# Kernel tuning notes

Hardware: AMD Instinct MI355X
Metric: run time of the kernel (lower is better)

Reference implementation:

```python
import jax, jax.numpy as jnp
import numpy as np

N_NODES = 100000
N_EDGES = 1600000
D_IN, D_HID, D_OUT = 256, 256, 128


def setup_inputs() -> dict:
    key = jax.random.key(0)
    k1, k2, k3, k4, k5, k6 = jax.random.split(key, 6)
    x = jax.random.normal(k1, (N_NODES, D_IN), dtype=jnp.float32)
    edge_index = jax.random.randint(k2, (2, N_EDGES), 0, N_NODES, dtype=jnp.int64)
    W1 = jax.random.normal(k3, (D_IN, D_HID), dtype=jnp.float32) / np.sqrt(D_IN)
    b1 = jax.random.normal(k4, (D_HID,), dtype=jnp.float32) * 0.01
    W2 = jax.random.normal(k5, (D_HID, D_OUT), dtype=jnp.float32) / np.sqrt(D_HID)
    b2 = jax.random.normal(k6, (D_OUT,), dtype=jnp.float32) * 0.01
    return {"x": x, "edge_index": edge_index, "W1": W1, "b1": b1, "W2": W2, "b2": b2}


def _gcn_conv(x, src, dst, W, b, n_nodes):
    # PyG GCNConv: linear transform, add self-loops, symmetric normalization,
    # scatter-add aggregation, bias.
    h = x @ W                                         # [N, D_out]
    # degree including self-loop (edge weight 1)
    deg = jax.ops.segment_sum(jnp.ones((src.shape[0],), h.dtype), dst,
                              num_segments=n_nodes) + 1.0
    dinv = jax.lax.rsqrt(deg)                         # [N]
    norm = dinv[src] * dinv[dst]                      # [E]
    msg = h[src] * norm[:, None]                      # [E, D_out] gather + scale
    agg = jax.ops.segment_sum(msg, dst, num_segments=n_nodes)
    # self-loop contribution: norm_ii = dinv_i^2
    agg = agg + h * (dinv * dinv)[:, None]
    return agg + b


def reference(x, edge_index, W1, b1, W2, b2):
    src, dst = edge_index[0], edge_index[1]
    n = x.shape[0]
    h = _gcn_conv(x, src, dst, W1, b1, n)
    h = jax.nn.relu(h)
    out = _gcn_conv(h, src, dst, W2, b2, n)
    return out
```

## Files before the change

kernel.cpp:

```cpp
#include <hip/hip_runtime.h>

#define N_NODES 100000
#define N_EDGES 1600000
#define D_IN 256
#define D_HID 256
#define D_OUT 128
#define SLOTS 96

typedef unsigned int u32;
typedef unsigned short u16;
typedef __attribute__((ext_vector_type(8))) short bf16x8;
typedef __attribute__((ext_vector_type(8))) unsigned short u16x8;
typedef __attribute__((ext_vector_type(4))) float f32x4;

__device__ __forceinline__ u16 f2bf(float v) {
    u32 u = __float_as_uint(v);
    u32 r = (u + 0x7fffu + ((u >> 16) & 1u)) >> 16;
    return (u16)r;
}
__device__ __forceinline__ float bf2f(u16 b) {
    return __uint_as_float(((u32)b) << 16);
}

__global__ __launch_bounds__(256) void prep_kernel(
    const float* __restrict__ x, u16* __restrict__ xhi,
    const float* __restrict__ W1, u16* __restrict__ w1hi, u16* __restrict__ w1lo,
    const float* __restrict__ W2, u16* __restrict__ w2hi, u16* __restrict__ w2lo,
    const int* __restrict__ src, const int* __restrict__ dst,
    int* __restrict__ deg, int* __restrict__ slot) {
    const int tid = blockIdx.x * 256 + threadIdx.x;
    const int stride = gridDim.x * 256;

    const int n4 = N_NODES * D_IN / 4;
    for (int i = tid; i < n4; i += stride) {
        const float4 v = ((const float4*)x)[i];
        ushort4 h;
        h.x = f2bf(v.x);
        h.y = f2bf(v.y);
        h.z = f2bf(v.z);
        h.w = f2bf(v.w);
        ((ushort4*)xhi)[i] = h;
    }
    for (int i = tid; i < D_IN * D_HID; i += stride) {
        const int k = i / D_HID, n = i - k * D_HID;
        const float v = W1[i];
        const u16 h = f2bf(v);
        w1hi[(size_t)n * D_IN + k] = h;
        w1lo[(size_t)n * D_IN + k] = f2bf(v - bf2f(h));
    }
    for (int i = tid; i < D_HID * D_OUT; i += stride) {
        const int k = i / D_OUT, n = i - k * D_OUT;
        const float v = W2[i];
        const u16 h = f2bf(v);
        w2hi[(size_t)n * D_HID + k] = h;
        w2lo[(size_t)n * D_HID + k] = f2bf(v - bf2f(h));
    }
    for (int e = tid; e < N_EDGES; e += stride) {
        const int s = src[e];
        const int d = dst[e];
        const int pos = atomicAdd(&deg[d], 1);
        if (pos < SLOTS) slot[(size_t)d * SLOTS + pos] = s;
    }
}

__global__ void dinv_kernel(const int* __restrict__ deg, float* __restrict__ dinv, int n) {
    int i = blockIdx.x * blockDim.x + threadIdx.x;
    if (i < n) dinv[i] = rsqrtf((float)deg[i] + 1.0f);
}

template <bool ASPLIT>
__global__ __launch_bounds__(256) void gemm_split(
    const u16* __restrict__ Ahi, const u16* __restrict__ Alo,
    const u16* __restrict__ Bhi, const u16* __restrict__ Blo,
    u16* __restrict__ Cb, int M, int N, int K) {
    constexpr int ABYTES = ASPLIT ? 16384 : 8192;
    __shared__ char lds[2][ABYTES + 16384];
    const int t = threadIdx.x;
    const int wave = t >> 6;
    const int lane = t & 63;
    const int wm = wave >> 1, wn = wave & 1;
    const int mBase = blockIdx.x * 128;
    const int nBase = blockIdx.y * 128;

    f32x4 acc[4][4];
#pragma unroll
    for (int i = 0; i < 4; ++i)
#pragma unroll
        for (int j = 0; j < 4; ++j) acc[i][j] = (f32x4){0.f, 0.f, 0.f, 0.f};

    const int lr = lane >> 3;
    const int lp = lane & 7;
    const int lc = lp ^ lr;
    const int lr4 = lane >> 2;
    const int lc4 = (lane & 3) ^ (lr4 & 3);

    auto STAGE = [&](int buf, int kt) {
        const int k0 = kt * 32;
        if (ASPLIT) {
            const int coff = k0 + (lc & 3) * 8;
            const u16* aSrc = (lc < 4) ? Ahi : Alo;
#pragma unroll
            for (int q = 0; q < 4; ++q) {
                const int row = wave * 32 + q * 8 + lr;
                int mg = mBase + row;
                if (mg > M - 1) mg = M - 1;
                const u16* s = aSrc + (size_t)mg * K + coff;
                char* d = &lds[buf][(wave * 32 + q * 8) * 128];
                __builtin_amdgcn_global_load_lds(
                    (const __attribute__((address_space(1))) u32*)s,
                    (__attribute__((address_space(3))) u32*)d, 16, 0, 0);
            }
        } else {
            const int coff = k0 + lc4 * 8;
#pragma unroll
            for (int q = 0; q < 2; ++q) {
                const int row = wave * 32 + q * 16 + lr4;
                int mg = mBase + row;
                if (mg > M - 1) mg = M - 1;
                const u16* s = Ahi + (size_t)mg * K + coff;
                char* d = &lds[buf][(wave * 32 + q * 16) * 64];
                __builtin_amdgcn_global_load_lds(
                    (const __attribute__((address_space(1))) u32*)s,
                    (__attribute__((address_space(3))) u32*)d, 16, 0, 0);
            }
        }
        {
            const int coff = k0 + (lc & 3) * 8;
            const u16* bSrc = (lc < 4) ? Bhi : Blo;
#pragma unroll
            for (int q = 0; q < 4; ++q) {
                const int row = wave * 32 + q * 8 + lr;
                const int ng = nBase + row;
                const u16* s = bSrc + (size_t)ng * K + coff;
                char* d = &lds[buf][ABYTES + (wave * 32 + q * 8) * 128];
                __builtin_amdgcn_global_load_lds(
                    (const __attribute__((address_space(1))) u32*)s,
                    (__attribute__((address_space(3))) u32*)d, 16, 0, 0);
            }
        }
    };

    auto COMPUTE = [&](int buf) {
        const char* pa = &lds[buf][0];
        const char* pb = &lds[buf][ABYTES];
        const int lm = lane & 15;
        const int c4 = lane >> 4;
        bf16x8 ah[4], al[4], bh[4], bl[4];
#pragma unroll
        for (int i = 0; i < 4; ++i) {
            const int r = wm * 64 + i * 16 + lm;
            if (ASPLIT) {
                const int s = r & 7;
                ah[i] = *(const bf16x8*)(pa + r * 128 + ((c4) ^ s) * 16);
                al[i] = *(const bf16x8*)(pa + r * 128 + ((c4 + 4) ^ s) * 16);
            } else {
                ah[i] = *(const bf16x8*)(pa + r * 64 + (c4 ^ (r & 3)) * 16);
            }
        }
#pragma unroll
        for (int j = 0; j < 4; ++j) {
            const int r = wn * 64 + j * 16 + lm;
            const int s = r & 7;
            bh[j] = *(const bf16x8*)(pb + r * 128 + ((c4) ^ s) * 16);
            bl[j] = *(const bf16x8*)(pb + r * 128 + ((c4 + 4) ^ s) * 16);
        }
#pragma unroll
        for (int i = 0; i < 4; ++i)
#pragma unroll
            for (int j = 0; j < 4; ++j)
                acc[i][j] = __builtin_amdgcn_mfma_f32_16x16x32_bf16(ah[i], bh[j], acc[i][j], 0, 0, 0);
#pragma unroll
        for (int i = 0; i < 4; ++i)
#pragma unroll
            for (int j = 0; j < 4; ++j)
                acc[i][j] = __builtin_amdgcn_mfma_f32_16x16x32_bf16(ah[i], bl[j], acc[i][j], 0, 0, 0);
        if (ASPLIT) {
#pragma unroll
            for (int i = 0; i < 4; ++i)
#pragma unroll
                for (int j = 0; j < 4; ++j)
                    acc[i][j] = __builtin_amdgcn_mfma_f32_16x16x32_bf16(al[i], bh[j], acc[i][j], 0, 0, 0);
        }
    };

    const int NT = K / 32;
    STAGE(0, 0);
#pragma unroll 1
    for (int kt = 0; kt < NT; ++kt) {
        __syncthreads();
        if (kt + 1 < NT) STAGE((kt + 1) & 1, kt + 1);
        COMPUTE(kt & 1);
        __syncthreads();
    }

    const int lm = lane & 15;
    const int c4 = lane >> 4;
#pragma unroll
    for (int i = 0; i < 4; ++i) {
#pragma unroll
        for (int r = 0; r < 4; ++r) {
            const int row = mBase + wm * 64 + i * 16 + c4 * 4 + r;
            if (row < M) {
#pragma unroll
                for (int j = 0; j < 4; ++j) {
                    const int col = nBase + wn * 64 + j * 16 + lm;
                    Cb[(size_t)row * N + col] = f2bf(acc[i][j][r]);
                }
            }
        }
    }
}

__global__ __launch_bounds__(256) void gather_agg_bf16(const u16* __restrict__ h,
                                                       const int* __restrict__ deg,
                                                       const int* __restrict__ slot,
                                                       const float* __restrict__ dinv,
                                                       const float* __restrict__ bias,
                                                       u16* __restrict__ ob, int n) {
    const int node = blockIdx.x * 8 + (threadIdx.x >> 5);
    const int lane = threadIdx.x & 31;
    if (node >= n) return;
    const float di = dinv[node];
    int dg = deg[node];
    if (dg > SLOTS) dg = SLOTS;
    const int* sp = &slot[(size_t)node * SLOTS];
    const int off = lane * 8;

    float acc[8];
#pragma unroll
    for (int j = 0; j < 8; ++j) acc[j] = 0.f;

    int k = 0;
    for (; k + 1 < dg; k += 2) {
        const int s0 = sp[k];
        const int s1 = sp[k + 1];
        const float n0 = dinv[s0] * di;
        const float n1 = dinv[s1] * di;
        const u16x8 va = *(const u16x8*)&h[(size_t)s0 * 256 + off];
        const u16x8 vb = *(const u16x8*)&h[(size_t)s1 * 256 + off];
#pragma unroll
        for (int j = 0; j < 8; ++j)
            acc[j] += bf2f(va[j]) * n0 + bf2f(vb[j]) * n1;
    }
    if (k < dg) {
        const int s0 = sp[k];
        const float n0 = dinv[s0] * di;
        const u16x8 va = *(const u16x8*)&h[(size_t)s0 * 256 + off];
#pragma unroll
        for (int j = 0; j < 8; ++j) acc[j] += bf2f(va[j]) * n0;
    }

    const float sl = di * di;
    const u16x8 hv = *(const u16x8*)&h[(size_t)node * 256 + off];
    const float4 bv0 = *(const float4*)&bias[off];
    const float4 bv1 = *(const float4*)&bias[off + 4];
    const float bb[8] = {bv0.x, bv0.y, bv0.z, bv0.w, bv1.x, bv1.y, bv1.z, bv1.w};
    u16x8 H;
#pragma unroll
    for (int j = 0; j < 8; ++j)
        H[j] = f2bf(fmaxf(acc[j] + bf2f(hv[j]) * sl + bb[j], 0.f));
    *(u16x8*)&ob[(size_t)node * 256 + off] = H;
}

__global__ __launch_bounds__(256) void gather_agg_out(const u16* __restrict__ h,
                                                      const int* __restrict__ deg,
                                                      const int* __restrict__ slot,
                                                      const float* __restrict__ dinv,
                                                      const float* __restrict__ bias,
                                                      float* __restrict__ outp, int n) {
    const int node = blockIdx.x * 16 + (threadIdx.x >> 4);
    const int lane = threadIdx.x & 15;
    if (node >= n) return;
    const float di = dinv[node];
    int dg = deg[node];
    if (dg > SLOTS) dg = SLOTS;
    const int* sp = &slot[(size_t)node * SLOTS];
    const int off = lane * 8;

    float acc[8];
#pragma unroll
    for (int j = 0; j < 8; ++j) acc[j] = 0.f;

    int k = 0;
    for (; k + 1 < dg; k += 2) {
        const int s0 = sp[k];
        const int s1 = sp[k + 1];
        const float n0 = dinv[s0] * di;
        const float n1 = dinv[s1] * di;
        const u16x8 va = *(const u16x8*)&h[(size_t)s0 * 128 + off];
        const u16x8 vb = *(const u16x8*)&h[(size_t)s1 * 128 + off];
#pragma unroll
        for (int j = 0; j < 8; ++j)
            acc[j] += bf2f(va[j]) * n0 + bf2f(vb[j]) * n1;
    }
    if (k < dg) {
        const int s0 = sp[k];
        const float n0 = dinv[s0] * di;
        const u16x8 va = *(const u16x8*)&h[(size_t)s0 * 128 + off];
#pragma unroll
        for (int j = 0; j < 8; ++j) acc[j] += bf2f(va[j]) * n0;
    }

    const float sl = di * di;
    const u16x8 hv = *(const u16x8*)&h[(size_t)node * 128 + off];
    const float4 bv0 = *(const float4*)&bias[off];
    const float4 bv1 = *(const float4*)&bias[off + 4];
    const float bb[8] = {bv0.x, bv0.y, bv0.z, bv0.w, bv1.x, bv1.y, bv1.z, bv1.w};
    float o[8];
#pragma unroll
    for (int j = 0; j < 8; ++j) o[j] = acc[j] + bf2f(hv[j]) * sl + bb[j];
    float4 o0 = make_float4(o[0], o[1], o[2], o[3]);
    float4 o1 = make_float4(o[4], o[5], o[6], o[7]);
    *(float4*)&outp[(size_t)node * 128 + off] = o0;
    *(float4*)&outp[(size_t)node * 128 + off + 4] = o1;
}

extern "C" void kernel_launch(void* const* d_in, const int* in_sizes, int n_in,
                              void* d_out, int out_size, void* d_ws, size_t ws_size,
                              hipStream_t stream) {
    const float* x  = (const float*)d_in[0];
    const int*   ei = (const int*)d_in[1];
    const float* W1 = (const float*)d_in[2];
    const float* b1 = (const float*)d_in[3];
    const float* W2 = (const float*)d_in[4];
    const float* b2 = (const float*)d_in[5];
    float* out = (float*)d_out;

    const int* src = ei;
    const int* dst = ei + N_EDGES;

    char* ws = (char*)d_ws;
    float* dinv = (float*)(ws + 0x000000);
    int*   deg  = (int*)  (ws + 0x080000);
    u16* wt1hi = (u16*)(ws + 0x200000);
    u16* wt1lo = (u16*)(ws + 0x220000);
    u16* wt2hi = (u16*)(ws + 0x240000);
    u16* wt2lo = (u16*)(ws + 0x250000);
    int* slot  = (int*)(ws + 0x280000);
    const size_t big = 0x2800000;
    u16*   Phi = (u16*)(ws + big);
    u16*   Hb  = (u16*)(ws + big + 51200000);

    hipMemsetAsync(deg, 0, N_NODES * sizeof(int), stream);

    prep_kernel<<<2048, 256, 0, stream>>>(x, Phi, W1, wt1hi, wt1lo,
                                          W2, wt2hi, wt2lo, src, dst, deg, slot);
    dinv_kernel<<<(N_NODES + 255) / 256, 256, 0, stream>>>(deg, dinv, N_NODES);

    {
        dim3 g((N_NODES + 127) / 128, D_HID / 128);
        gemm_split<false><<<g, 256, 0, stream>>>(Phi, (const u16*)nullptr, wt1hi, wt1lo,
                                                 Hb, N_NODES, D_HID, D_IN);
    }
    gather_agg_bf16<<<(N_NODES + 7) / 8, 256, 0, stream>>>(
        Hb, deg, slot, dinv, b1, Phi, N_NODES);

    {
        dim3 g((N_NODES + 127) / 128, D_OUT / 128);
        gemm_split<false><<<g, 256, 0, stream>>>(Phi, (const u16*)nullptr, wt2hi, wt2lo,
                                                 Hb, N_NODES, D_OUT, D_HID);
    }
    gather_agg_out<<<(N_NODES + 15) / 16, 256, 0, stream>>>(
        Hb, deg, slot, dinv, b2, out, N_NODES);
}
```

Measured before the change: 375.4 us.

## Bin edges by destination bucket before slot scatter to localize atomics

Edge-to-slot construction moves out of the prep kernel into a two-pass scheme. Edges are first binned into 1024 destination buckets using shared-memory histograms and one global offset per bucket. A per-bucket kernel then does the degree atomics and slot writes, so they hit a compact node range instead of random addresses across all nodes. It adds two launches, an extra pass over the edges through a binned buffer, and a per-bucket cap of 2048 that could drop edges if a bucket overflows. The unused ASPLIT template path is removed from the GEMM.

```diff
diff --git a/kernel.cpp b/kernel.cpp
--- a/kernel.cpp
+++ b/kernel.cpp
@@ -7,6 +7,11 @@
 #define D_OUT 128
 #define SLOTS 96
 
+#define NB 1024
+#define NPB 98
+#define CAP 2048
+#define BIN_T 8192
+
 typedef unsigned int u32;
 typedef unsigned short u16;
 typedef __attribute__((ext_vector_type(8))) short bf16x8;
@@ -25,9 +30,7 @@
 __global__ __launch_bounds__(256) void prep_kernel(
     const float* __restrict__ x, u16* __restrict__ xhi,
     const float* __restrict__ W1, u16* __restrict__ w1hi, u16* __restrict__ w1lo,
-    const float* __restrict__ W2, u16* __restrict__ w2hi, u16* __restrict__ w2lo,
-    const int* __restrict__ src, const int* __restrict__ dst,
-    int* __restrict__ deg, int* __restrict__ slot) {
+    const float* __restrict__ W2, u16* __restrict__ w2hi, u16* __restrict__ w2lo) {
     const int tid = blockIdx.x * 256 + threadIdx.x;
     const int stride = gridDim.x * 256;
 
@@ -55,11 +58,56 @@
         w2hi[(size_t)n * D_HID + k] = h;
         w2lo[(size_t)n * D_HID + k] = f2bf(v - bf2f(h));
     }
-    for (int e = tid; e < N_EDGES; e += stride) {
-        const int s = src[e];
-        const int d = dst[e];
-        const int pos = atomicAdd(&deg[d], 1);
-        if (pos < SLOTS) slot[(size_t)d * SLOTS + pos] = s;
+}
+
+__global__ __launch_bounds__(256) void bin_kernel(const int* __restrict__ src,
+                                                  const int* __restrict__ dst,
+                                                  int* __restrict__ gcnt,
+                                                  int2* __restrict__ binned, int E) {
+    __shared__ int hist[NB];
+    __shared__ int cur[NB];
+    const int t = threadIdx.x;
+    const int base = blockIdx.x * BIN_T;
+#pragma unroll
+    for (int q = 0; q < NB / 256; ++q) hist[q * 256 + t] = 0;
+    __syncthreads();
+#pragma unroll 4
+    for (int j = 0; j < BIN_T / 256; ++j) {
+        const int e = base + j * 256 + t;
+        if (e < E) atomicAdd(&hist[dst[e] / NPB], 1);
+    }
+    __syncthreads();
+#pragma unroll
+    for (int q = 0; q < NB / 256; ++q) {
+        const int b = q * 256 + t;
+        const int c = hist[b];
+        cur[b] = c ? atomicAdd(&gcnt[b], c) : 0;
+    }
+    __syncthreads();
+#pragma unroll 4
+    for (int j = 0; j < BIN_T / 256; ++j) {
+        const int e = base + j * 256 + t;
+        if (e < E) {
+            const int d = dst[e];
+            const int b = d / NPB;
+            const int r = atomicAdd(&cur[b], 1);
+            if (r < CAP) binned[(size_t)b * CAP + r] = make_int2(src[e], d);
+        }
+    }
+}
+
+__global__ __launch_bounds__(256) void bucket_scatter(const int* __restrict__ gcnt,
+                                                      const int2* __restrict__ binned,
+                                                      int* __restrict__ deg,
+                                                      int* __restrict__ slot) {
+    const int b = blockIdx.x;
+    int cnt = gcnt[b];
+    if (cnt > CAP) cnt = CAP;
+    const int2* ep = &binned[(size_t)b * CAP];
+    for (int i = threadIdx.x; i < cnt; i += 256) {
+        const int2 e = ep[i];
+        const int pos = atomicAdd(&deg[e.y], 1);
+        if (pos < SLOTS) slot[(size_t)e.y * SLOTS + pos] = e.x;
     }
 }
 
@@ -68,12 +116,11 @@
     if (i < n) dinv[i] = rsqrtf((float)deg[i] + 1.0f);
 }
 
-template <bool ASPLIT>
 __global__ __launch_bounds__(256) void gemm_split(
-    const u16* __restrict__ Ahi, const u16* __restrict__ Alo,
+    const u16* __restrict__ Ahi,
     const u16* __restrict__ Bhi, const u16* __restrict__ Blo,
     u16* __restrict__ Cb, int M, int N, int K) {
-    constexpr int ABYTES = ASPLIT ? 16384 : 8192;
+    constexpr int ABYTES = 8192;
     __shared__ char lds[2][ABYTES + 16384];
     const int t = threadIdx.x;
     const int wave = t >> 6;
@@ -96,21 +143,7 @@
 
     auto STAGE = [&](int buf, int kt) {
         const int k0 = kt * 32;
-        if (ASPLIT) {
-            const int coff = k0 + (lc & 3) * 8;
-            const u16* aSrc = (lc < 4) ? Ahi : Alo;
-#pragma unroll
-            for (int q = 0; q < 4; ++q) {
-                const int row = wave * 32 + q * 8 + lr;
-                int mg = mBase + row;
-                if (mg > M - 1) mg = M - 1;
-                const u16* s = aSrc + (size_t)mg * K + coff;
-                char* d = &lds[buf][(wave * 32 + q * 8) * 128];
-                __builtin_amdgcn_global_load_lds(
-                    (const __attribute__((address_space(1))) u32*)s,
-                    (__attribute__((address_space(3))) u32*)d, 16, 0, 0);
-            }
-        } else {
+        {
             const int coff = k0 + lc4 * 8;
 #pragma unroll
             for (int q = 0; q < 2; ++q) {
@@ -145,17 +178,11 @@
         const char* pb = &lds[buf][ABYTES];
         const int lm = lane & 15;
         const int c4 = lane >> 4;
-        bf16x8 ah[4], al[4], bh[4], bl[4];
+        bf16x8 ah[4], bh[4], bl[4];
 #pragma unroll
         for (int i = 0; i < 4; ++i) {
             const int r = wm * 64 + i * 16 + lm;
-            if (ASPLIT) {
-                const int s = r & 7;
-                ah[i] = *(const bf16x8*)(pa + r * 128 + ((c4) ^ s) * 16);
-                al[i] = *(const bf16x8*)(pa + r * 128 + ((c4 + 4) ^ s) * 16);
-            } else {
-                ah[i] = *(const bf16x8*)(pa + r * 64 + (c4 ^ (r & 3)) * 16);
-            }
+            ah[i] = *(const bf16x8*)(pa + r * 64 + (c4 ^ (r & 3)) * 16);
         }
 #pragma unroll
         for (int j = 0; j < 4; ++j) {
@@ -174,13 +201,6 @@
 #pragma unroll
             for (int j = 0; j < 4; ++j)
                 acc[i][j] = __builtin_amdgcn_mfma_f32_16x16x32_bf16(ah[i], bl[j], acc[i][j], 0, 0, 0);
-        if (ASPLIT) {
-#pragma unroll
-            for (int i = 0; i < 4; ++i)
-#pragma unroll
-                for (int j = 0; j < 4; ++j)
-                    acc[i][j] = __builtin_amdgcn_mfma_f32_16x16x32_bf16(al[i], bh[j], acc[i][j], 0, 0, 0);
-        }
     };
 
     const int NT = K / 32;
@@ -332,33 +352,35 @@
     char* ws = (char*)d_ws;
     float* dinv = (float*)(ws + 0x000000);
     int*   deg  = (int*)  (ws + 0x080000);
+    int*   gcnt = (int*)  (ws + 0x100000);
     u16* wt1hi = (u16*)(ws + 0x200000);
     u16* wt1lo = (u16*)(ws + 0x220000);
     u16* wt2hi = (u16*)(ws + 0x240000);
     u16* wt2lo = (u16*)(ws + 0x250000);
-    int* slot  = (int*)(ws + 0x280000);
-    const size_t big = 0x2800000;
-    u16*   Phi = (u16*)(ws + big);
-    u16*   Hb  = (u16*)(ws + big + 51200000);
+    int2* binned = (int2*)(ws + 0x280000);
+    int*  slot   = (int*) (ws + 0x1300000);
+    const size_t big = 0x3800000;
+    u16* Phi = (u16*)(ws + big);
+    u16* Hb  = (u16*)(ws + big + 51200000);
 
     hipMemsetAsync(deg, 0, N_NODES * sizeof(int), stream);
-
-    prep_kernel<<<2048, 256, 0, stream>>>(x, Phi, W1, wt1hi, wt1lo,
-                                          W2, wt2hi, wt2lo, src, dst, deg, slot);
+    hipMemsetAsync(gcnt, 0, NB * sizeof(int), stream);
+
+    prep_kernel<<<2048, 256, 0, stream>>>(x, Phi, W1, wt1hi, wt1lo, W2, wt2hi, wt2lo);
+    bin_kernel<<<(N_EDGES + BIN_T - 1) / BIN_T, 256, 0, stream>>>(src, dst, gcnt, binned, N_EDGES);
+    bucket_scatter<<<NB, 256, 0, stream>>>(gcnt, binned, deg, slot);
     dinv_kernel<<<(N_NODES + 255) / 256, 256, 0, stream>>>(deg, dinv, N_NODES);
 
     {
         dim3 g((N_NODES + 127) / 128, D_HID / 128);
-        gemm_split<false><<<g, 256, 0, stream>>>(Phi, (const u16*)nullptr, wt1hi, wt1lo,
-                                                 Hb, N_NODES, D_HID, D_IN);
+        gemm_split<<<g, 256, 0, stream>>>(Phi, wt1hi, wt1lo, Hb, N_NODES, D_HID, D_IN);
     }
     gather_agg_bf16<<<(N_NODES + 7) / 8, 256, 0, stream>>>(
         Hb, deg, slot, dinv, b1, Phi, N_NODES);
 
     {
         dim3 g((N_NODES + 127) / 128, D_OUT / 128);
-        gemm_split<false><<<g, 256, 0, stream>>>(Phi, (const u16*)nullptr, wt2hi, wt2lo,
-                                                 Hb, N_NODES, D_OUT, D_HID);
+        gemm_split<<<g, 256, 0, stream>>>(Phi, wt2hi, wt2lo, Hb, N_NODES, D_OUT, D_HID);
     }
     gather_agg_out<<<(N_NODES + 15) / 16, 256, 0, stream>>>(
         Hb, deg, slot, dinv, b2, out, N_NODES);
```

New measurement: 381.9 us. No clear change (+1.7%).
